# Kernel tuning notes

Measured on AMD Instinct MI355X. Metric: run time of the kernel, lower is better.

Reference implementation:

```python
import jax, jax.numpy as jnp
import numpy as np

N = 16_000_000   # total interaction rows
U = 160_000      # number of users (segments)
K = 10           # NDCG cutoff (top_k)
SAMPLE_FRAC = 0.3


def setup_inputs() -> dict:
    key = jax.random.key(0)
    k1, k2, k3 = jax.random.split(key, 3)
    predictions = jax.random.normal(k1, (N,), dtype=jnp.float32)
    targets = jax.random.uniform(k2, (N,), dtype=jnp.float32)
    indexes = jax.random.randint(k3, (N,), 0, U).astype(jnp.int32)
    return {"predictions": predictions, "targets": targets, "indexes": indexes}


def _ndcg_per_user(predictions, targets, indexes):
    n = predictions.shape[0]
    # segment sizes and start offsets (indexes need not be pre-sorted)
    counts = jax.ops.segment_sum(jnp.ones(n, jnp.int32), indexes, num_segments=U)
    starts = jnp.cumsum(counts) - counts  # [U]

    pos = jnp.arange(n, dtype=jnp.int32)

    def topk_weights(scores):
        # stable segmented descending sort: primary key = user id, secondary = -score
        order = jnp.lexsort((-scores, indexes))  # [N]
        s_idx = indexes[order]
        rank = pos - starts[s_idx]  # within-segment rank, 0-based
        # discount 1/log2(rank+2), zero beyond top-k
        w = jnp.where(rank < K,
                      1.0 / jnp.log2(rank.astype(jnp.float32) + 2.0),
                      0.0)
        return order, s_idx, w

    order_p, sidx_p, w_p = topk_weights(predictions)
    dcg = jax.ops.segment_sum(targets[order_p] * w_p, sidx_p, num_segments=U)

    order_t, sidx_t, w_t = topk_weights(targets)
    idcg = jax.ops.segment_sum(targets[order_t] * w_t, sidx_t, num_segments=U)

    ndcg = jnp.where(idcg > 0, dcg / jnp.maximum(idcg, 1e-12), 0.0)  # [U]
    present = counts > 0
    return ndcg, present


def reference(predictions, targets, indexes):
    ndcg, present = _ndcg_per_user(predictions, targets, indexes)
    # With N >> U every user is present w.h.p., so sampling over all U ids
    # matches sampling over unique present users.
    n_sampled = max(1, int(SAMPLE_FRAC * U))
    perm = jax.random.permutation(jax.random.key(42), U)
    sampled = jnp.zeros((U,), dtype=bool).at[perm[:n_sampled]].set(True)
    mask = sampled & present
    denom = jnp.maximum(jnp.sum(mask).astype(jnp.float32), 1.0)
    return jnp.sum(jnp.where(mask, ndcg, 0.0)) / denom
```

## Files before the change

### kernel.cpp

```cpp
#include <hip/hip_runtime.h>
#include <hip/hip_fp16.h>

#define U_SEG 160000
#define TOPK 10
#define NBLK 504
#define CHUNK4 8323
#define NBINS 625
#define UPB 256
#define SCAN_N (NBINS * NBLK)
#define SCAN_BLK 154

#define NCHUNK 252
#define CHUNKC (2 * CHUNK4)
#define NRNDC 17
#define GBINS 313
#define BUFD 48
#define NBPG 5

#define NDCG_BLKS 1250
#define UPH 128
#define CAP_HALF 13824
#define MSTR 81

__global__ __launch_bounds__(1024)
void k_hist(const int4* __restrict__ idx4, int n4, int* __restrict__ histmat,
            float* __restrict__ accum) {
  if (blockIdx.x == 0 && threadIdx.x == 0) {
    atomicExch((int*)accum + 0, 0);
    atomicExch((int*)accum + 1, 0);
    atomicExch((int*)accum + 2, 0);
  }
  __shared__ int h[NBINS];
  for (int t = threadIdx.x; t < NBINS; t += 1024) h[t] = 0;
  __syncthreads();
  int k = blockIdx.x;
  int beg = k * CHUNK4;
  int end = beg + CHUNK4; if (end > n4) end = n4;
  for (int i = beg + threadIdx.x; i < end; i += 1024) {
    int4 u = idx4[i];
    atomicAdd(&h[u.x >> 8], 1);
    atomicAdd(&h[u.y >> 8], 1);
    atomicAdd(&h[u.z >> 8], 1);
    atomicAdd(&h[u.w >> 8], 1);
  }
  __syncthreads();
  for (int t = threadIdx.x; t < NBINS; t += 1024)
    histmat[t * NBLK + k] = h[t];
}

__global__ void k_scan1(const int* __restrict__ in, int* __restrict__ out,
                        int* __restrict__ bsums, int m) {
  int t = threadIdx.x;
  int base = blockIdx.x * 2048 + t * 8;
  int v[8]; int s = 0;
#pragma unroll
  for (int j = 0; j < 8; j++) { v[j] = (base + j < m) ? in[base + j] : 0; s += v[j]; }
  int lane = t & 63, wv = t >> 6;
  int incl = s;
#pragma unroll
  for (int off = 1; off < 64; off <<= 1) {
    int tmp = __shfl_up(incl, off);
    if (lane >= off) incl += tmp;
  }
  __shared__ int wsum[4];
  if (lane == 63) wsum[wv] = incl;
  __syncthreads();
  int woff = 0;
  for (int w = 0; w < wv; w++) woff += wsum[w];
  int excl = woff + incl - s;
#pragma unroll
  for (int j = 0; j < 8; j++) {
    if (base + j < m) out[base + j] = excl;
    excl += v[j];
  }
  if (t == 255) bsums[blockIdx.x] = excl;
}

__global__ void k_scan3(int* __restrict__ out, const int* __restrict__ bsums, int m) {
  __shared__ int sh[4];
  __shared__ int addsh;
  int tid = threadIdx.x;
  int nb = blockIdx.x;
  int v = 0;
  for (int j = tid; j < nb; j += 256) v += bsums[j];
#pragma unroll
  for (int off = 32; off > 0; off >>= 1) v += __shfl_xor(v, off);
  if ((tid & 63) == 0) sh[tid >> 6] = v;
  __syncthreads();
  if (tid == 0) addsh = sh[0] + sh[1] + sh[2] + sh[3];
  __syncthreads();
  int add = addsh;
  int base = blockIdx.x * 2048 + tid * 8;
#pragma unroll
  for (int j = 0; j < 8; j++)
    if (base + j < m) out[base + j] += add;
}

__global__ __launch_bounds__(1024, 8)
void k_scatter(const float4* __restrict__ pred4, const float4* __restrict__ tgt4,
               const int4* __restrict__ idx4, int n4,
               const int* __restrict__ starts,
               unsigned* __restrict__ keys, unsigned char* __restrict__ uidb) {
  __shared__ unsigned kbuf[GBINS][BUFD];
  __shared__ unsigned char ubuf[GBINS][BUFD];
  __shared__ int gbase[GBINS];
  __shared__ int fill[GBINS];

  int bid = blockIdx.x;
  int x = bid & 7;
  int L = x * 63 + (bid >> 3);
  int c = L >> 1;
  int g = L & 1;
  int lo = g * 313;
  int nb = g ? 312 : 313;

  int tid = threadIdx.x;
  int lane = tid & 63, wv = tid >> 6;
  int grp = lane >> 4;
  int r16 = lane & 15;
  int gid = wv * 4 + grp;

  for (int t = tid; t < nb; t += 1024) {
    gbase[t] = starts[(lo + t) * NBLK + 2 * c];
    fill[t] = 0;
  }
  __syncthreads();

  int beg = c * CHUNKC;
  int end = beg + CHUNKC; if (end > n4) end = n4;

  int i = beg + tid;
  bool have = (i < end);
  float4 p = {0.f, 0.f, 0.f, 0.f}, t4 = {0.f, 0.f, 0.f, 0.f};
  int4 u = {0, 0, 0, 0};
  if (have) { p = pred4[i]; t4 = tgt4[i]; u = idx4[i]; }

  for (int rr = 0; rr < NRNDC; ++rr) {
    int inext = beg + (rr + 1) * 1024 + tid;
    bool hn = (rr + 1 < NRNDC) && (inext < end);
    float4 pn = {0.f, 0.f, 0.f, 0.f}, tn = {0.f, 0.f, 0.f, 0.f};
    int4 un = {0, 0, 0, 0};
    if (hn) { pn = pred4[inext]; tn = tgt4[inext]; un = idx4[inext]; }

    if (have) {
#pragma unroll
      for (int e = 0; e < 4; e++) {
        int uu = (e == 0) ? u.x : (e == 1) ? u.y : (e == 2) ? u.z : u.w;
        int bb = (uu >> 8) - lo;
        if ((unsigned)bb < (unsigned)nb) {
          float pp = (e == 0) ? p.x : (e == 1) ? p.y : (e == 2) ? p.z : p.w;
          float tt = (e == 0) ? t4.x : (e == 1) ? t4.y : (e == 2) ? t4.z : t4.w;
          unsigned int up = (unsigned int)__half_as_ushort(__float2half_rn(pp));
          unsigned int mp = up ^ ((up >> 15) ? 0xFFFFu : 0x8000u);
          unsigned int ut = (unsigned int)__half_as_ushort(__float2half_rn(tt));
          unsigned key = (mp << 16) | ut;
          unsigned char ub = (unsigned char)(uu & 255);
          int s = atomicAdd(&fill[bb], 1);
          if (s < BUFD) { kbuf[bb][s] = key; ubuf[bb][s] = ub; }
          else { int gb = gbase[bb]; keys[gb + s] = key; uidb[gb + s] = ub; }
        }
      }
    }
    asm volatile("s_waitcnt lgkmcnt(0)" ::: "memory");
    __builtin_amdgcn_s_barrier();

    int fv[NBPG], gv[NBPG];
#pragma unroll
    for (int j = 0; j < NBPG; j++) {
      int b = gid + 64 * j;
      bool ok = (b < nb);
      fv[j] = ok ? fill[b] : 0;
      gv[j] = ok ? gbase[b] : 0;
    }
#pragma unroll
    for (int j = 0; j < NBPG; j++) {
      int b = gid + 64 * j;
      if (b >= nb) continue;
      int f = fv[j];
      int gb = gv[j];
      if (f > BUFD) {
        keys[gb + r16] = kbuf[b][r16];
        keys[gb + 16 + r16] = kbuf[b][16 + r16];
        keys[gb + 32 + r16] = kbuf[b][32 + r16];
        uidb[gb + r16] = ubuf[b][r16];
        uidb[gb + 16 + r16] = ubuf[b][16 + r16];
        uidb[gb + 32 + r16] = ubuf[b][32 + r16];
        if (r16 == 0) { fill[b] = 0; gbase[b] = gb + f; }
      } else if (f >= 32) {
        unsigned k0 = kbuf[b][r16];
        unsigned k1 = kbuf[b][16 + r16];
        unsigned char u0 = ubuf[b][r16];
        unsigned char u1 = ubuf[b][16 + r16];
        int r = f - 32;
        unsigned mk = 0u; unsigned char mu = 0;
        bool mv = (r16 < r);
        if (mv) { mk = kbuf[b][32 + r16]; mu = ubuf[b][32 + r16]; }
        keys[gb + r16] = k0;
        keys[gb + 16 + r16] = k1;
        uidb[gb + r16] = u0;
        uidb[gb + 16 + r16] = u1;
        if (mv) { kbuf[b][r16] = mk; ubuf[b][r16] = mu; }
        if (r16 == 0) { fill[b] = r; gbase[b] = gb + 32; }
      }
    }
    asm volatile("s_waitcnt lgkmcnt(0)" ::: "memory");
    __builtin_amdgcn_s_barrier();

    p = pn; t4 = tn; u = un; have = hn; i = inext;
  }

  {
    int fv[NBPG], gv[NBPG];
#pragma unroll
    for (int j = 0; j < NBPG; j++) {
      int b = gid + 64 * j;
      bool ok = (b < nb);
      fv[j] = ok ? fill[b] : 0;
      gv[j] = ok ? gbase[b] : 0;
    }
#pragma unroll
    for (int j = 0; j < NBPG; j++) {
      int b = gid + 64 * j;
      if (b >= nb) continue;
      int f = fv[j];
      int gb = gv[j];
      if (r16 < f) { keys[gb + r16] = kbuf[b][r16]; uidb[gb + r16] = ubuf[b][r16]; }
      if (16 + r16 < f) { keys[gb + 16 + r16] = kbuf[b][16 + r16]; uidb[gb + 16 + r16] = ubuf[b][16 + r16]; }
    }
  }
}

__device__ __forceinline__ void insert10(unsigned (&k)[TOPK], unsigned w) {
  bool ba[TOPK];
#pragma unroll
  for (int j = 0; j < TOPK; j++) ba[j] = w > k[j];
#pragma unroll
  for (int j = TOPK - 1; j >= 1; --j)
    k[j] = ba[j] ? (ba[j - 1] ? k[j - 1] : w) : k[j];
  k[0] = ba[0] ? w : k[0];
}

__global__ __launch_bounds__(1024, 8)
void k_ndcg(const unsigned* __restrict__ keys, const unsigned char* __restrict__ uidb,
            const int* __restrict__ starts, int n, float* __restrict__ accum,
            float* __restrict__ outp) {
  __shared__ int cnt[UPH];
  __shared__ int ust[UPH];
  __shared__ int ucur[UPH];
  __shared__ unsigned int fine[CAP_HALF];
  __shared__ int wsum[2];
  __shared__ float wred[2];
  __shared__ int wredc[2];

  const float disc[TOPK] = {1.0f, 0.6309297535714574f, 0.5f, 0.4306765580733931f,
                            0.38685280723454163f, 0.35620718710802255f, 0.3333333333333333f,
                            0.31546487678572877f, 0.30102999566398114f, 0.2890648263178878f};
  int b = blockIdx.x, tid = threadIdx.x;
  int lane = tid & 63, wv = tid >> 6;
  int pb = b >> 1;
  unsigned hb = (unsigned)((b & 1) << 7);

  int pstart = starts[pb * NBLK];
  int pend = (pb == NBINS - 1) ? n : starts[(pb + 1) * NBLK];

  if (tid < UPH) cnt[tid] = 0;
  __syncthreads();

  int i = pstart + tid;
  for (; i + 3072 < pend; i += 4096) {
    unsigned a0 = uidb[i];
    unsigned a1 = uidb[i + 1024];
    unsigned a2 = uidb[i + 2048];
    unsigned a3 = uidb[i + 3072];
    if ((a0 & 128u) == hb) atomicAdd(&cnt[a0 & 127u], 1);
    if ((a1 & 128u) == hb) atomicAdd(&cnt[a1 & 127u], 1);
    if ((a2 & 128u) == hb) atomicAdd(&cnt[a2 & 127u], 1);
    if ((a3 & 128u) == hb) atomicAdd(&cnt[a3 & 127u], 1);
  }
  for (; i < pend; i += 1024) {
    unsigned a = uidb[i];
    if ((a & 128u) == hb) atomicAdd(&cnt[a & 127u], 1);
  }
  __syncthreads();

  if (tid < UPH) {
    int v = cnt[tid], incl = v;
#pragma unroll
    for (int off = 1; off < 64; off <<= 1) {
      int tmp = __shfl_up(incl, off);
      if (lane >= off) incl += tmp;
    }
    if (lane == 63) wsum[wv] = incl;
  }
  __syncthreads();
  if (tid < UPH) {
    int v = cnt[tid], incl = v;
#pragma unroll
    for (int off = 1; off < 64; off <<= 1) {
      int tmp = __shfl_up(incl, off);
      if (lane >= off) incl += tmp;
    }
    int e = (wv ? wsum[0] : 0) + incl - v;
    ust[tid] = e; ucur[tid] = e;
  }
  __syncthreads();

  i = pstart + tid;
  for (; i + 3072 < pend; i += 4096) {
    unsigned a0 = uidb[i];
    unsigned a1 = uidb[i + 1024];
    unsigned a2 = uidb[i + 2048];
    unsigned a3 = uidb[i + 3072];
    unsigned k0 = keys[i];
    unsigned k1 = keys[i + 1024];
    unsigned k2 = keys[i + 2048];
    unsigned k3 = keys[i + 3072];
    if ((a0 & 128u) == hb) { int p = atomicAdd(&ucur[a0 & 127u], 1); if (p < CAP_HALF) fine[p] = k0; }
    if ((a1 & 128u) == hb) { int p = atomicAdd(&ucur[a1 & 127u], 1); if (p < CAP_HALF) fine[p] = k1; }
    if ((a2 & 128u) == hb) { int p = atomicAdd(&ucur[a2 & 127u], 1); if (p < CAP_HALF) fine[p] = k2; }
    if ((a3 & 128u) == hb) { int p = atomicAdd(&ucur[a3 & 127u], 1); if (p < CAP_HALF) fine[p] = k3; }
  }
  for (; i < pend; i += 1024) {
    unsigned a = uidb[i];
    unsigned k0 = keys[i];
    if ((a & 128u) == hb) { int p = atomicAdd(&ucur[a & 127u], 1); if (p < CAP_HALF) fine[p] = k0; }
  }
  __syncthreads();

  int u = tid & 127, part = tid >> 7;
  unsigned kA[TOPK], kB[TOPK];
#pragma unroll
  for (int j = 0; j < TOPK; j++) { kA[j] = 0u; kB[j] = 0u; }
  {
    int c = cnt[u], base = ust[u];
    int ie = base + c; if (ie > CAP_HALF) ie = CAP_HALF;
    for (int t2 = base + part; t2 < ie; t2 += 8) {
      unsigned w = fine[t2];
      unsigned y = w & 0xFFFFu;
      insert10(kA, w);
      insert10(kB, y);
    }
  }
  __syncthreads();

#pragma unroll
  for (int j = 0; j < TOPK; j++) fine[u * MSTR + part * TOPK + j] = kA[j];
  __syncthreads();
  float dcg = 0.f;
  if (tid < UPH) {
    int pr[8];
#pragma unroll
    for (int p = 0; p < 8; p++) pr[p] = 0;
#pragma unroll
    for (int j = 0; j < TOPK; j++) {
      unsigned best = 0u; int bp = 0;
#pragma unroll
      for (int p = 0; p < 8; p++) {
        unsigned v = fine[tid * MSTR + p * TOPK + pr[p]];
        if (v > best) { best = v; bp = p; }
      }
#pragma unroll
      for (int p = 0; p < 8; p++) pr[p] += (bp == p) ? 1 : 0;
      dcg += __half2float(__ushort_as_half((unsigned short)(best & 0xFFFFu))) * disc[j];
    }
  }
  __syncthreads();
#pragma unroll
  for (int j = 0; j < TOPK; j++) fine[u * MSTR + part * TOPK + j] = kB[j];
  __syncthreads();
  if (tid < UPH) {
    int pr[8];
#pragma unroll
    for (int p = 0; p < 8; p++) pr[p] = 0;
    float idcg = 0.f;
#pragma unroll
    for (int j = 0; j < TOPK; j++) {
      unsigned best = 0u; int bp = 0;
#pragma unroll
      for (int p = 0; p < 8; p++) {
        unsigned v = fine[tid * MSTR + p * TOPK + pr[p]];
        if (v > best) { best = v; bp = p; }
      }
#pragma unroll
      for (int p = 0; p < 8; p++) pr[p] += (bp == p) ? 1 : 0;
      idcg += __half2float(__ushort_as_half((unsigned short)best)) * disc[j];
    }
    float nd = (idcg > 0.f) ? dcg / fmaxf(idcg, 1e-12f) : 0.f;
    int have = (cnt[tid] > 0) ? 1 : 0;
#pragma unroll
    for (int off = 32; off > 0; off >>= 1) {
      nd += __shfl_xor(nd, off);
      have += __shfl_xor(have, off);
    }
    if (lane == 0) { wred[wv] = nd; wredc[wv] = have; }
  }
  __syncthreads();
  if (tid == 0) {
    atomicAdd(&accum[0], wred[0] + wred[1]);
    atomicAdd((int*)accum + 1, wredc[0] + wredc[1]);
    __threadfence();
    int old = atomicAdd((int*)accum + 2, 1);
    if (old == NDCG_BLKS - 1) {
      __threadfence();
      float s = atomicAdd(&accum[0], 0.0f);
      int cc = atomicAdd((int*)accum + 1, 0);
      outp[0] = s / fmaxf((float)cc, 1.0f);
    }
  }
}

extern "C" void kernel_launch(void* const* d_in, const int* in_sizes, int n_in,
                              void* d_out, int out_size, void* d_ws, size_t ws_size,
                              hipStream_t stream) {
  int n = in_sizes[0];
  const float* pred = (const float*)d_in[0];
  const float* tgt = (const float*)d_in[1];
  const int* idx = (const int*)d_in[2];
  float* out = (float*)d_out;

  char* base = (char*)d_ws;
  unsigned* keys = (unsigned*)base;
  unsigned char* uidb = (unsigned char*)(base + (size_t)n * 4);
  int* histmat = (int*)(base + (size_t)n * 5);
  int* starts = histmat + SCAN_N;
  int* bsums = starts + SCAN_N;
  float* accum = (float*)(bsums + ((SCAN_BLK + 63) & ~63));

  size_t need = (size_t)n * 5
              + ((size_t)2 * SCAN_N + ((SCAN_BLK + 63) & ~63) + 16) * sizeof(int);
  if (ws_size < need) return;

  int n4 = n >> 2;
  k_hist<<<NBLK, 1024, 0, stream>>>((const int4*)idx, n4, histmat, accum);
  k_scan1<<<SCAN_BLK, 256, 0, stream>>>(histmat, starts, bsums, SCAN_N);
  k_scan3<<<SCAN_BLK, 256, 0, stream>>>(starts, bsums, SCAN_N);
  k_scatter<<<NBLK, 1024, 0, stream>>>((const float4*)pred, (const float4*)tgt,
                                       (const int4*)idx, n4, starts, keys, uidb);
  k_ndcg<<<NDCG_BLKS, 1024, 0, stream>>>(keys, uidb, starts, n, accum, out);
}
```

Baseline: 366.7 us.

## Privatize histogram, process two rows per scatter round, vectorize uid count loads

The histogram kernel now keeps two shared-memory histograms split by thread parity and handles two int4 loads per iteration, which cuts LDS atomic contention and raises load parallelism. The scatter kernel processes two 1024-row slices per barrier round instead of one and halves the round count, dropping the register prefetch pipeline. This halves the barrier and flush passes per chunk but puts up to twice as many entries into each shared bin buffer between flushes, so more of them spill to direct global writes. The NDCG count pass reads user bytes as uchar4 with aligned head and tail handling to cut the number of load instructions.

```diff
diff --git a/kernel.cpp b/kernel.cpp
--- a/kernel.cpp
+++ b/kernel.cpp
@@ -12,7 +12,7 @@
 
 #define NCHUNK 252
 #define CHUNKC (2 * CHUNK4)
-#define NRNDC 17
+#define NRNDC 9
 #define GBINS 313
 #define BUFD 48
 #define NBPG 5
@@ -30,22 +30,30 @@
     atomicExch((int*)accum + 1, 0);
     atomicExch((int*)accum + 2, 0);
   }
-  __shared__ int h[NBINS];
-  for (int t = threadIdx.x; t < NBINS; t += 1024) h[t] = 0;
+  __shared__ int h0[NBINS], h1[NBINS];
+  for (int t = threadIdx.x; t < NBINS; t += 1024) { h0[t] = 0; h1[t] = 0; }
   __syncthreads();
   int k = blockIdx.x;
   int beg = k * CHUNK4;
   int end = beg + CHUNK4; if (end > n4) end = n4;
-  for (int i = beg + threadIdx.x; i < end; i += 1024) {
-    int4 u = idx4[i];
-    atomicAdd(&h[u.x >> 8], 1);
-    atomicAdd(&h[u.y >> 8], 1);
-    atomicAdd(&h[u.z >> 8], 1);
-    atomicAdd(&h[u.w >> 8], 1);
+  int* h = (threadIdx.x & 1) ? h1 : h0;
+  int i = beg + threadIdx.x;
+  for (; i + 1024 < end; i += 2048) {
+    int4 a = idx4[i];
+    int4 b = idx4[i + 1024];
+    atomicAdd(&h[a.x >> 8], 1); atomicAdd(&h[a.y >> 8], 1);
+    atomicAdd(&h[a.z >> 8], 1); atomicAdd(&h[a.w >> 8], 1);
+    atomicAdd(&h[b.x >> 8], 1); atomicAdd(&h[b.y >> 8], 1);
+    atomicAdd(&h[b.z >> 8], 1); atomicAdd(&h[b.w >> 8], 1);
+  }
+  if (i < end) {
+    int4 a = idx4[i];
+    atomicAdd(&h[a.x >> 8], 1); atomicAdd(&h[a.y >> 8], 1);
+    atomicAdd(&h[a.z >> 8], 1); atomicAdd(&h[a.w >> 8], 1);
   }
   __syncthreads();
   for (int t = threadIdx.x; t < NBINS; t += 1024)
-    histmat[t * NBLK + k] = h[t];
+    histmat[t * NBLK + k] = h0[t] + h1[t];
 }
 
 __global__ void k_scan1(const int* __restrict__ in, int* __restrict__ out,
@@ -129,38 +137,39 @@
   int beg = c * CHUNKC;
   int end = beg + CHUNKC; if (end > n4) end = n4;
 
-  int i = beg + tid;
-  bool have = (i < end);
-  float4 p = {0.f, 0.f, 0.f, 0.f}, t4 = {0.f, 0.f, 0.f, 0.f};
-  int4 u = {0, 0, 0, 0};
-  if (have) { p = pred4[i]; t4 = tgt4[i]; u = idx4[i]; }
+#define PLACE_ROW(HV, UU, PP, TT)                                              \
+  if (HV) {                                                                    \
+    _Pragma("unroll")                                                          \
+    for (int e = 0; e < 4; e++) {                                              \
+      int uu = (e == 0) ? UU.x : (e == 1) ? UU.y : (e == 2) ? UU.z : UU.w;     \
+      int bb = (uu >> 8) - lo;                                                 \
+      if ((unsigned)bb < (unsigned)nb) {                                       \
+        float pp = (e == 0) ? PP.x : (e == 1) ? PP.y : (e == 2) ? PP.z : PP.w; \
+        float tt = (e == 0) ? TT.x : (e == 1) ? TT.y : (e == 2) ? TT.z : TT.w; \
+        unsigned up = (unsigned)__half_as_ushort(__float2half_rn(pp));         \
+        unsigned mp = up ^ ((up >> 15) ? 0xFFFFu : 0x8000u);                   \
+        unsigned ut = (unsigned)__half_as_ushort(__float2half_rn(tt));         \
+        unsigned key = (mp << 16) | ut;                                        \
+        unsigned char ub = (unsigned char)(uu & 255);                          \
+        int s = atomicAdd(&fill[bb], 1);                                       \
+        if (s < BUFD) { kbuf[bb][s] = key; ubuf[bb][s] = ub; }                 \
+        else { int gb = gbase[bb]; keys[gb + s] = key; uidb[gb + s] = ub; }    \
+      }                                                                        \
+    }                                                                          \
+  }
 
   for (int rr = 0; rr < NRNDC; ++rr) {
-    int inext = beg + (rr + 1) * 1024 + tid;
-    bool hn = (rr + 1 < NRNDC) && (inext < end);
-    float4 pn = {0.f, 0.f, 0.f, 0.f}, tn = {0.f, 0.f, 0.f, 0.f};
-    int4 un = {0, 0, 0, 0};
-    if (hn) { pn = pred4[inext]; tn = tgt4[inext]; un = idx4[inext]; }
-
-    if (have) {
-#pragma unroll
-      for (int e = 0; e < 4; e++) {
-        int uu = (e == 0) ? u.x : (e == 1) ? u.y : (e == 2) ? u.z : u.w;
-        int bb = (uu >> 8) - lo;
-        if ((unsigned)bb < (unsigned)nb) {
-          float pp = (e == 0) ? p.x : (e == 1) ? p.y : (e == 2) ? p.z : p.w;
-          float tt = (e == 0) ? t4.x : (e == 1) ? t4.y : (e == 2) ? t4.z : t4.w;
-          unsigned int up = (unsigned int)__half_as_ushort(__float2half_rn(pp));
-          unsigned int mp = up ^ ((up >> 15) ? 0xFFFFu : 0x8000u);
-          unsigned int ut = (unsigned int)__half_as_ushort(__float2half_rn(tt));
-          unsigned key = (mp << 16) | ut;
-          unsigned char ub = (unsigned char)(uu & 255);
-          int s = atomicAdd(&fill[bb], 1);
-          if (s < BUFD) { kbuf[bb][s] = key; ubuf[bb][s] = ub; }
-          else { int gb = gbase[bb]; keys[gb + s] = key; uidb[gb + s] = ub; }
-        }
-      }
-    }
+    int i0 = beg + rr * 2048 + tid;
+    int i1 = i0 + 1024;
+    bool hA = (i0 < end), hB = (i1 < end);
+    float4 pA = {0,0,0,0}, tA = {0,0,0,0}, pB = {0,0,0,0}, tB = {0,0,0,0};
+    int4 uA = {0,0,0,0}, uB = {0,0,0,0};
+    if (hA) { pA = pred4[i0]; tA = tgt4[i0]; uA = idx4[i0]; }
+    if (hB) { pB = pred4[i1]; tB = tgt4[i1]; uB = idx4[i1]; }
+
+    PLACE_ROW(hA, uA, pA, tA)
+    PLACE_ROW(hB, uB, pB, tB)
+
     asm volatile("s_waitcnt lgkmcnt(0)" ::: "memory");
     __builtin_amdgcn_s_barrier();
 
@@ -205,9 +214,8 @@
     }
     asm volatile("s_waitcnt lgkmcnt(0)" ::: "memory");
     __builtin_amdgcn_s_barrier();
-
-    p = pn; t4 = tn; u = un; have = hn; i = inext;
-  }
+  }
+#undef PLACE_ROW
 
   {
     int fv[NBPG], gv[NBPG];
@@ -266,20 +274,26 @@
   if (tid < UPH) cnt[tid] = 0;
   __syncthreads();
 
-  int i = pstart + tid;
-  for (; i + 3072 < pend; i += 4096) {
-    unsigned a0 = uidb[i];
-    unsigned a1 = uidb[i + 1024];
-    unsigned a2 = uidb[i + 2048];
-    unsigned a3 = uidb[i + 3072];
-    if ((a0 & 128u) == hb) atomicAdd(&cnt[a0 & 127u], 1);
-    if ((a1 & 128u) == hb) atomicAdd(&cnt[a1 & 127u], 1);
-    if ((a2 & 128u) == hb) atomicAdd(&cnt[a2 & 127u], 1);
-    if ((a3 & 128u) == hb) atomicAdd(&cnt[a3 & 127u], 1);
-  }
-  for (; i < pend; i += 1024) {
-    unsigned a = uidb[i];
-    if ((a & 128u) == hb) atomicAdd(&cnt[a & 127u], 1);
+  {
+    int a4beg = (pstart + 3) & ~3;
+    if (a4beg > pend) a4beg = pend;
+    if (tid < a4beg - pstart) {
+      unsigned a = uidb[pstart + tid];
+      if ((a & 128u) == hb) atomicAdd(&cnt[a & 127u], 1);
+    }
+    for (int w = a4beg + tid * 4; w + 3 < pend; w += 4096) {
+      uchar4 cc = *reinterpret_cast<const uchar4*>(uidb + w);
+      unsigned a0 = cc.x, a1 = cc.y, a2 = cc.z, a3 = cc.w;
+      if ((a0 & 128u) == hb) atomicAdd(&cnt[a0 & 127u], 1);
+      if ((a1 & 128u) == hb) atomicAdd(&cnt[a1 & 127u], 1);
+      if ((a2 & 128u) == hb) atomicAdd(&cnt[a2 & 127u], 1);
+      if ((a3 & 128u) == hb) atomicAdd(&cnt[a3 & 127u], 1);
+    }
+    int rem = (pend > a4beg) ? ((pend - a4beg) & 3) : 0;
+    if (tid < rem) {
+      unsigned a = uidb[pend - rem + tid];
+      if ((a & 128u) == hb) atomicAdd(&cnt[a & 127u], 1);
+    }
   }
   __syncthreads();
 
@@ -305,7 +319,7 @@
   }
   __syncthreads();
 
-  i = pstart + tid;
+  int i = pstart + tid;
   for (; i + 3072 < pend; i += 4096) {
     unsigned a0 = uidb[i];
     unsigned a1 = uidb[i + 1024];
```

Result: no change. 365.2 us (-0.4%).
